# Kernel tuning notes

Hardware: AMD Instinct MI355X
Metric: run time of the kernel (lower is better)

Reference implementation:

```python
import jax, jax.numpy as jnp
import numpy as np

N = 50000          # nodes
E = 1_600_000      # edges (avg degree 32)
D_IN = 128
D_OUT = 128
K = 16             # SSGC hops
ALPHA = 0.05


def setup_inputs() -> dict:
    key = jax.random.key(0)
    k1, k2, k3 = jax.random.split(key, 3)
    node_emb = jax.random.normal(k1, (N, D_IN), dtype=jnp.float32)
    edge_index = jax.random.randint(k2, (2, E), 0, N, dtype=jnp.int32)
    # Parameters of SSGConv's internal Linear(in_channels, out_channels)
    weight = jax.random.normal(k3, (D_OUT, D_IN), dtype=jnp.float32) * (1.0 / np.sqrt(D_IN))
    bias = jnp.zeros((D_OUT,), dtype=jnp.float32)
    return {"node_emb": node_emb, "edge_index": edge_index, "weight": weight, "bias": bias}


def reference(node_emb, edge_index, weight, bias):
    n = node_emb.shape[0]
    # GCN normalization with self-loops (PyG gcn_norm, add_self_loops=True)
    loops = jnp.arange(n, dtype=edge_index.dtype)
    src = jnp.concatenate([edge_index[0], loops])  # [E+N]
    dst = jnp.concatenate([edge_index[1], loops])  # [E+N]
    ones = jnp.ones(src.shape[0], dtype=node_emb.dtype)
    deg = jax.ops.segment_sum(ones, dst, num_segments=n)           # in-degree incl. self-loop
    dinv = jnp.where(deg > 0, jax.lax.rsqrt(deg), 0.0)
    norm = dinv[src] * dinv[dst]                                   # [E+N]

    def prop(x):
        msgs = norm[:, None] * x[src]                              # [E+N, D]
        return jax.ops.segment_sum(msgs, dst, num_segments=n)

    # SSGConv: h = alpha*x0 + (1-alpha)/K * sum_{k=1..K} A_hat^k x0, then Linear
    def step(carry, _):
        x, h = carry
        x = prop(x)
        h = h + ((1.0 - ALPHA) / K) * x
        return (x, h), None

    (_, h), _ = jax.lax.scan(step, (node_emb, ALPHA * node_emb), None, length=K)
    out = h @ weight.T + bias
    # Dropout(p=0.5) is identity in eval mode
    return out
```

## Files before the change

### kernel.cpp

```cpp
#include <hip/hip_runtime.h>


#define N_NODES 50000
#define N_EDGES 1600000
#define D 128
#define K_HOPS 16
#define ALPHA 0.05f
#define HCOEF ((1.0f - ALPHA) / (float)K_HOPS)
#define NREP 8
#define N_SBLK ((N_NODES + 255) / 256)

#define DEG_IPT 8
#define REP_OF(i) (((i) >> 11) & (NREP - 1))

__device__ __forceinline__ unsigned int f2bf(float f) {
    unsigned int u = __float_as_uint(f);
    return (u + 0x7FFFu + ((u >> 16) & 1u)) >> 16;
}
__device__ __forceinline__ unsigned int pack_bf2(float x, float y) {
    return f2bf(x) | (f2bf(y) << 16);
}
__device__ __forceinline__ float bf_lo(unsigned int w) { return __uint_as_float(w << 16); }
__device__ __forceinline__ float bf_hi(unsigned int w) { return __uint_as_float(w & 0xFFFF0000u); }

__global__ void deg_kernel(const int* __restrict__ dst, int* __restrict__ degR,
                           int* __restrict__ rank, int e) {
    int gid = blockIdx.x * 256 + threadIdx.x;
    int i0 = gid * DEG_IPT;
    if (i0 >= e) return;
    int rep = REP_OF(i0);
    int* base = degR + rep * N_NODES;
    int4 d0 = *(const int4*)&dst[i0];
    int4 d1 = *(const int4*)&dst[i0 + 4];
    int r[8];
    r[0] = atomicAdd(&base[d0.x], 1);
    r[1] = atomicAdd(&base[d0.y], 1);
    r[2] = atomicAdd(&base[d0.z], 1);
    r[3] = atomicAdd(&base[d0.w], 1);
    r[4] = atomicAdd(&base[d1.x], 1);
    r[5] = atomicAdd(&base[d1.y], 1);
    r[6] = atomicAdd(&base[d1.z], 1);
    r[7] = atomicAdd(&base[d1.w], 1);
    *(int4*)&rank[i0]     = make_int4(r[0], r[1], r[2], r[3]);
    *(int4*)&rank[i0 + 4] = make_int4(r[4], r[5], r[6], r[7]);
}

__global__ void combine_kernel(int* __restrict__ degR, int* __restrict__ deg,
                               float* __restrict__ dinv, float* __restrict__ selfw, int n) {
    int i = blockIdx.x * 256 + threadIdx.x;
    if (i < n) {
        int run = 0;
        #pragma unroll
        for (int r = 0; r < NREP; ++r) {
            int v = degR[r * N_NODES + i];
            degR[r * N_NODES + i] = run;
            run += v;
        }
        deg[i] = run;
        float di = rsqrtf((float)(run + 1));
        dinv[i] = di;
        selfw[i] = di * di;
    }
}

__device__ __forceinline__ int block_scan_excl(int v) {
    __shared__ int ws[4];
    int tid = threadIdx.x, lane = tid & 63, wid = tid >> 6;
    int s = v;
    #pragma unroll
    for (int off = 1; off < 64; off <<= 1) {
        int t = __shfl_up(s, off, 64);
        if (lane >= off) s += t;
    }
    if (lane == 63) ws[wid] = s;
    __syncthreads();
    int woff = 0;
    #pragma unroll
    for (int w = 0; w < 3; ++w)
        if (w < wid) woff += ws[w];
    return woff + s - v;
}

__global__ void scan_part(const int* __restrict__ deg, int* __restrict__ part, int n) {
    int i = blockIdx.x * 256 + threadIdx.x;
    int v = (i < n) ? deg[i] : 0;
    #pragma unroll
    for (int off = 1; off < 64; off <<= 1) v += __shfl_xor(v, off, 64);
    __shared__ int ws[4];
    if ((threadIdx.x & 63) == 0) ws[threadIdx.x >> 6] = v;
    __syncthreads();
    if (threadIdx.x == 0) part[blockIdx.x] = ws[0] + ws[1] + ws[2] + ws[3];
}

__global__ void scan_mid(int* __restrict__ part, int nb) {
    int tid = threadIdx.x;
    int v = (tid < nb) ? part[tid] : 0;
    int e = block_scan_excl(v);
    if (tid < nb) part[tid] = e;
}

__global__ void scan_fin(const int* __restrict__ deg, const int* __restrict__ part,
                         int* __restrict__ row_start, int n) {
    int i = blockIdx.x * 256 + threadIdx.x;
    int v = (i < n) ? deg[i] : 0;
    int e = block_scan_excl(v) + part[blockIdx.x];
    if (i < n) row_start[i] = e;
    if (i == n - 1) row_start[n] = e + v;
}

__global__ void scatter_kernel(const int* __restrict__ src, const int* __restrict__ dst,
                               const int* __restrict__ rank, const int* __restrict__ row_start,
                               const int* __restrict__ pref, int2* __restrict__ csr,
                               const float* __restrict__ dinv, int e) {
    int gid = blockIdx.x * 256 + threadIdx.x;
    int i0 = gid * 4;
    if (i0 >= e) return;
    int4 dv = *(const int4*)&dst[i0];
    int4 sv = *(const int4*)&src[i0];
    int4 rv = *(const int4*)&rank[i0];
    int d[4] = {dv.x, dv.y, dv.z, dv.w};
    int s[4] = {sv.x, sv.y, sv.z, sv.w};
    int r[4] = {rv.x, rv.y, rv.z, rv.w};
    int pos[4];
    float w[4];
    #pragma unroll
    for (int q = 0; q < 4; ++q) {
        int rep = REP_OF(i0 + q);
        pos[q] = row_start[d[q]] + pref[rep * N_NODES + d[q]] + r[q];
        w[q] = dinv[d[q]] * dinv[s[q]];
    }
    #pragma unroll
    for (int q = 0; q < 4; ++q)
        csr[pos[q]] = make_int2(s[q], __float_as_int(w[q]));
}

__global__ void init_kernel(const float2* __restrict__ x0, unsigned int* __restrict__ xb,
                            float2* __restrict__ h, int n2) {
    int i = blockIdx.x * blockDim.x + threadIdx.x;
    if (i < n2) {
        float2 v = x0[i];
        xb[i] = pack_bf2(v.x, v.y);
        h[i] = make_float2(ALPHA * v.x, ALPHA * v.y);
    }
}

#define GATHER_BLOCK(W)                                                         \
    {                                                                           \
        unsigned int g[W];                                                      \
        float wv[W];                                                            \
        _Pragma("unroll") for (int q = 0; q < W; ++q) {                         \
            int s = __shfl(rec.x, j + q);                                       \
            wv[q] = __int_as_float(__shfl(rec.y, j + q));                       \
            g[q] = xb[(size_t)s * 64 + lane];                                   \
        }                                                                       \
        _Pragma("unroll") for (int q = 0; q < W; ++q) {                         \
            accx += wv[q] * bf_lo(g[q]);                                        \
            accy += wv[q] * bf_hi(g[q]);                                        \
        }                                                                       \
        j += W;                                                                 \
    }

__global__ __launch_bounds__(256) void agg_kernel(
    const unsigned int* __restrict__ xb, unsigned int* __restrict__ yb,
    float2* __restrict__ h2, const float* __restrict__ selfw,
    const int* __restrict__ row_start, const int2* __restrict__ csr, int update_h) {
    int wid = threadIdx.x >> 6;
    int lane = threadIdx.x & 63;
    int node = blockIdx.x * 4 + wid;
    if (node >= N_NODES) return;

    int r0 = row_start[node];
    int r1 = row_start[node + 1];
    int deg = r1 - r0;
    size_t o = (size_t)node * 64 + lane;

    unsigned int vw = xb[o];
    float sw = selfw[node];
    float accx = sw * bf_lo(vw), accy = sw * bf_hi(vw);

    for (int base = 0; base < deg; base += 64) {
        int cnt = deg - base;
        if (cnt > 64) cnt = 64;
        int idx = r0 + base + lane;
        if (idx >= r1) idx = r1 - 1;
        int2 rec = csr[idx];

        int j = 0;
        while (j + 16 <= cnt) GATHER_BLOCK(16);
        if (j + 8 <= cnt) GATHER_BLOCK(8);
        if (j + 4 <= cnt) GATHER_BLOCK(4);
        for (; j < cnt; ++j) {
            int s = __shfl(rec.x, j);
            float w = __int_as_float(__shfl(rec.y, j));
            unsigned int gw = xb[(size_t)s * 64 + lane];
            accx += w * bf_lo(gw);
            accy += w * bf_hi(gw);
        }
    }

    yb[o] = pack_bf2(accx, accy);
    if (update_h) {
        float2 hv = h2[o];
        hv.x += HCOEF * (bf_lo(vw) + accx);
        hv.y += HCOEF * (bf_hi(vw) + accy);
        h2[o] = hv;
    }
}

__global__ __launch_bounds__(256) void gemm_kernel(
    const float* __restrict__ h, const float* __restrict__ w,
    const float* __restrict__ bias, float* __restrict__ out) {
    __shared__ float sAT[128][64];
    __shared__ float sBT[128][64];
    int tid = threadIdx.x;
    int row0 = blockIdx.x * 64;
    int col0 = blockIdx.y * 64;

    for (int idx = tid; idx < 64 * 32; idx += 256) {
        int r = idx & 63, kq = idx >> 6;
        float4 v;
        if (row0 + r < N_NODES)
            v = *(const float4*)&h[(size_t)(row0 + r) * D + kq * 4];
        else
            v = make_float4(0.f, 0.f, 0.f, 0.f);
        sAT[kq * 4 + 0][r] = v.x;
        sAT[kq * 4 + 1][r] = v.y;
        sAT[kq * 4 + 2][r] = v.z;
        sAT[kq * 4 + 3][r] = v.w;
    }
    for (int idx = tid; idx < 64 * 32; idx += 256) {
        int c = idx & 63, kq = idx >> 6;
        float4 v = *(const float4*)&w[(size_t)(col0 + c) * D + kq * 4];
        sBT[kq * 4 + 0][c] = v.x;
        sBT[kq * 4 + 1][c] = v.y;
        sBT[kq * 4 + 2][c] = v.z;
        sBT[kq * 4 + 3][c] = v.w;
    }
    __syncthreads();

    int cg = tid & 15;
    int rg = tid >> 4;
    float acc[4][4] = {};
    #pragma unroll 2
    for (int k = 0; k < 128; ++k) {
        float4 a = *(const float4*)&sAT[k][rg * 4];
        float4 b = *(const float4*)&sBT[k][cg * 4];
        acc[0][0] += a.x * b.x; acc[0][1] += a.x * b.y; acc[0][2] += a.x * b.z; acc[0][3] += a.x * b.w;
        acc[1][0] += a.y * b.x; acc[1][1] += a.y * b.y; acc[1][2] += a.y * b.z; acc[1][3] += a.y * b.w;
        acc[2][0] += a.z * b.x; acc[2][1] += a.z * b.y; acc[2][2] += a.z * b.z; acc[2][3] += a.z * b.w;
        acc[3][0] += a.w * b.x; acc[3][1] += a.w * b.y; acc[3][2] += a.w * b.z; acc[3][3] += a.w * b.w;
    }

    float4 bv = *(const float4*)&bias[col0 + cg * 4];
    #pragma unroll
    for (int i = 0; i < 4; ++i) {
        int r = row0 + rg * 4 + i;
        if (r < N_NODES) {
            float4 ov = make_float4(acc[i][0] + bv.x, acc[i][1] + bv.y,
                                    acc[i][2] + bv.z, acc[i][3] + bv.w);
            *(float4*)&out[(size_t)r * D + col0 + cg * 4] = ov;
        }
    }
}

extern "C" void kernel_launch(void* const* d_in, const int* in_sizes, int n_in,
                              void* d_out, int out_size, void* d_ws, size_t ws_size,
                              hipStream_t stream) {
    const float* node_emb = (const float*)d_in[0];
    const int*   edge     = (const int*)d_in[1];
    const float* weight   = (const float*)d_in[2];
    const float* bias     = (const float*)d_in[3];
    float* out = (float*)d_out;

    char* ws = (char*)d_ws;
    float*        hbuf = (float*)ws;        ws += (size_t)N_NODES * D * sizeof(float);
    unsigned int* xb0  = (unsigned int*)ws; ws += (size_t)N_NODES * 64 * sizeof(unsigned int);
    unsigned int* xb1  = (unsigned int*)ws; ws += (size_t)N_NODES * 64 * sizeof(unsigned int);
    int2*  csr      = (int2*)ws;  ws += (size_t)N_EDGES * sizeof(int2);
    int*   rank     = (int*)ws;   ws += (size_t)N_EDGES * sizeof(int);
    int*   degR     = (int*)ws;   ws += (size_t)NREP * N_NODES * sizeof(int);
    int*   deg      = (int*)ws;   ws += (size_t)N_NODES * sizeof(int);
    int*   row_start= (int*)ws;   ws += (size_t)(N_NODES + 16) * sizeof(int);
    float* dinv     = (float*)ws; ws += (size_t)N_NODES * sizeof(float);
    float* selfw    = (float*)ws; ws += (size_t)N_NODES * sizeof(float);
    int*   part     = (int*)ws;   ws += 256 * sizeof(int);

    const int* srcp = edge;
    const int* dstp = edge + N_EDGES;

    hipMemsetAsync(degR, 0, (size_t)NREP * N_NODES * sizeof(int), stream);

    int deg_threads = N_EDGES / DEG_IPT;
    deg_kernel<<<(deg_threads + 255) / 256, 256, 0, stream>>>(dstp, degR, rank, N_EDGES);
    combine_kernel<<<(N_NODES + 255) / 256, 256, 0, stream>>>(degR, deg, dinv, selfw, N_NODES);
    scan_part<<<N_SBLK, 256, 0, stream>>>(deg, part, N_NODES);
    scan_mid<<<1, 256, 0, stream>>>(part, N_SBLK);
    scan_fin<<<N_SBLK, 256, 0, stream>>>(deg, part, row_start, N_NODES);
    int sc_threads = N_EDGES / 4;
    scatter_kernel<<<(sc_threads + 255) / 256, 256, 0, stream>>>(srcp, dstp, rank, row_start,
                                                                 degR, csr, dinv, N_EDGES);

    int n2 = N_NODES * D / 2;
    init_kernel<<<(n2 + 255) / 256, 256, 0, stream>>>((const float2*)node_emb, xb0,
                                                      (float2*)hbuf, n2);

    unsigned int* cur = xb0;
    unsigned int* nxt = xb1;
    for (int k = 0; k < K_HOPS; ++k) {
        agg_kernel<<<(N_NODES + 3) / 4, 256, 0, stream>>>(cur, nxt, (float2*)hbuf,
                                                          selfw, row_start, csr, k & 1);
        unsigned int* tmp = cur; cur = nxt; nxt = tmp;
    }

    dim3 ggrid((N_NODES + 63) / 64, 2);
    gemm_kernel<<<ggrid, 256, 0, stream>>>(hbuf, weight, bias, out);
}
```

Before: 1.072 ms.

## Restructure aggregation to 16-lane groups handling four nodes across column slices

The aggregation kernel no longer gives each node a full 64-lane wavefront. Each 16-lane group now processes four consecutive nodes, looping over four 16-word column slices, with shuffles of width 16 and a reduced grid. The aim is to cut wasted lanes and shuffle overhead and to raise memory-level parallelism per wave. In exchange, each gathered row is read as 64-byte segments across four separate passes, and each lane does four times as much sequential work, which may lower achieved bandwidth.

Result: slower. 2.022 ms (+88.6%).

```diff
diff --git a/kernel.cpp b/kernel.cpp
--- a/kernel.cpp
+++ b/kernel.cpp
@@ -12,6 +12,11 @@
 
 #define DEG_IPT 8
 #define REP_OF(i) (((i) >> 11) & (NREP - 1))
+
+#define GROUPS_PER_BLOCK 16
+#define N_GROUPS (N_NODES / 4)
+#define AGG_BLOCKS ((N_GROUPS + GROUPS_PER_BLOCK - 1) / GROUPS_PER_BLOCK)
+#define N_SLICES 4
 
 __device__ __forceinline__ unsigned int f2bf(float f) {
     unsigned int u = __float_as_uint(f);
@@ -144,18 +149,18 @@
     }
 }
 
-#define GATHER_BLOCK(W)                                                         \
+#define GATHER_G(W)                                                             \
     {                                                                           \
-        unsigned int g[W];                                                      \
+        unsigned int gg[W];                                                     \
         float wv[W];                                                            \
         _Pragma("unroll") for (int q = 0; q < W; ++q) {                         \
-            int s = __shfl(rec.x, j + q);                                       \
-            wv[q] = __int_as_float(__shfl(rec.y, j + q));                       \
-            g[q] = xb[(size_t)s * 64 + lane];                                   \
+            int ss = __shfl(rec.x, j + q, 16);                                  \
+            wv[q] = __int_as_float(__shfl(rec.y, j + q, 16));                   \
+            gg[q] = xb[(size_t)ss * 64 + soff];                                 \
         }                                                                       \
         _Pragma("unroll") for (int q = 0; q < W; ++q) {                         \
-            accx += wv[q] * bf_lo(g[q]);                                        \
-            accy += wv[q] * bf_hi(g[q]);                                        \
+            accx += wv[q] * bf_lo(gg[q]);                                       \
+            accy += wv[q] * bf_hi(gg[q]);                                       \
         }                                                                       \
         j += W;                                                                 \
     }
@@ -164,46 +169,51 @@
     const unsigned int* __restrict__ xb, unsigned int* __restrict__ yb,
     float2* __restrict__ h2, const float* __restrict__ selfw,
     const int* __restrict__ row_start, const int2* __restrict__ csr, int update_h) {
-    int wid = threadIdx.x >> 6;
-    int lane = threadIdx.x & 63;
-    int node = blockIdx.x * 4 + wid;
-    if (node >= N_NODES) return;
-
-    int r0 = row_start[node];
-    int r1 = row_start[node + 1];
-    int deg = r1 - r0;
-    size_t o = (size_t)node * 64 + lane;
-
-    unsigned int vw = xb[o];
-    float sw = selfw[node];
-    float accx = sw * bf_lo(vw), accy = sw * bf_hi(vw);
-
-    for (int base = 0; base < deg; base += 64) {
-        int cnt = deg - base;
-        if (cnt > 64) cnt = 64;
-        int idx = r0 + base + lane;
-        if (idx >= r1) idx = r1 - 1;
-        int2 rec = csr[idx];
-
-        int j = 0;
-        while (j + 16 <= cnt) GATHER_BLOCK(16);
-        if (j + 8 <= cnt) GATHER_BLOCK(8);
-        if (j + 4 <= cnt) GATHER_BLOCK(4);
-        for (; j < cnt; ++j) {
-            int s = __shfl(rec.x, j);
-            float w = __int_as_float(__shfl(rec.y, j));
-            unsigned int gw = xb[(size_t)s * 64 + lane];
-            accx += w * bf_lo(gw);
-            accy += w * bf_hi(gw);
+    int g = blockIdx.x * GROUPS_PER_BLOCK + (threadIdx.x >> 4);
+    int sub = threadIdx.x & 15;
+    if (g >= N_GROUPS) return;
+    int n0 = g * 4;
+
+    for (int s = 0; s < N_SLICES; ++s) {
+        int soff = s * 16 + sub;
+        #pragma unroll
+        for (int ni = 0; ni < 4; ++ni) {
+            int node = n0 + ni;
+            int r0 = row_start[node];
+            int r1 = row_start[node + 1];
+            size_t o = (size_t)node * 64 + soff;
+
+            unsigned int vw = xb[o];
+            float sw = selfw[node];
+            float accx = sw * bf_lo(vw), accy = sw * bf_hi(vw);
+
+            for (int base = r0; base < r1; base += 16) {
+                int cnt = r1 - base;
+                if (cnt > 16) cnt = 16;
+                int idx = base + sub;
+                if (idx >= r1) idx = r1 - 1;
+                int2 rec = csr[idx];
+
+                int j = 0;
+                while (j + 8 <= cnt) GATHER_G(8);
+                if (j + 4 <= cnt) GATHER_G(4);
+                for (; j < cnt; ++j) {
+                    int ss = __shfl(rec.x, j, 16);
+                    float w = __int_as_float(__shfl(rec.y, j, 16));
+                    unsigned int gw = xb[(size_t)ss * 64 + soff];
+                    accx += w * bf_lo(gw);
+                    accy += w * bf_hi(gw);
+                }
+            }
+
+            yb[o] = pack_bf2(accx, accy);
+            if (update_h) {
+                float2 hv = h2[o];
+                hv.x += HCOEF * (bf_lo(vw) + accx);
+                hv.y += HCOEF * (bf_hi(vw) + accy);
+                h2[o] = hv;
+            }
         }
-    }
-
-    yb[o] = pack_bf2(accx, accy);
-    if (update_h) {
-        float2 hv = h2[o];
-        hv.x += HCOEF * (bf_lo(vw) + accx);
-        hv.y += HCOEF * (bf_hi(vw) + accy);
-        h2[o] = hv;
     }
 }
 
@@ -307,8 +317,8 @@
     unsigned int* cur = xb0;
     unsigned int* nxt = xb1;
     for (int k = 0; k < K_HOPS; ++k) {
-        agg_kernel<<<(N_NODES + 3) / 4, 256, 0, stream>>>(cur, nxt, (float2*)hbuf,
-                                                          selfw, row_start, csr, k & 1);
+        agg_kernel<<<AGG_BLOCKS, 256, 0, stream>>>(cur, nxt, (float2*)hbuf,
+                                                   selfw, row_start, csr, k & 1);
         unsigned int* tmp = cur; cur = nxt; nxt = tmp;
     }
 
```

## Slice bf16 feature matrix into four 64-byte column slices for gather locality

Applied to the files above, without the earlier changes.

The bf16 node features are stored as four column slices of 32 dims each, so each slice of the whole graph is 50000 x 64 bytes. The aggregation grid runs slice by slice, so the working set of one pass stays small enough to live in cache. Within a wavefront, four 16-lane groups each process different edges, and a cross-lane reduction combines them at the end. The edge list is now read four times per hop, and nontemporal loads and stores are added for the CSR, output and h traffic.

New measurement: 1.792 ms. 1.67x slower.

```diff
diff --git a/kernel.cpp b/kernel.cpp
--- a/kernel.cpp
+++ b/kernel.cpp
@@ -12,6 +12,10 @@
 
 #define DEG_IPT 8
 #define REP_OF(i) (((i) >> 11) & (NREP - 1))
+
+#define N_SLICES 4
+#define SLICE_STRIDE ((size_t)N_NODES * 16)
+#define BLOCKS_PER_SLICE (N_NODES / 4)
 
 __device__ __forceinline__ unsigned int f2bf(float f) {
     unsigned int u = __float_as_uint(f);
@@ -134,76 +138,99 @@
         csr[pos[q]] = make_int2(s[q], __float_as_int(w[q]));
 }
 
-__global__ void init_kernel(const float2* __restrict__ x0, unsigned int* __restrict__ xb,
+__global__ void init_kernel(const float2* __restrict__ x0, unsigned int* __restrict__ xbs,
                             float2* __restrict__ h, int n2) {
     int i = blockIdx.x * blockDim.x + threadIdx.x;
     if (i < n2) {
         float2 v = x0[i];
-        xb[i] = pack_bf2(v.x, v.y);
+        int node = i >> 6, d = i & 63;
+        int slice = d >> 4, sub = d & 15;
+        xbs[(size_t)slice * SLICE_STRIDE + (size_t)node * 16 + sub] = pack_bf2(v.x, v.y);
         h[i] = make_float2(ALPHA * v.x, ALPHA * v.y);
     }
 }
 
-#define GATHER_BLOCK(W)                                                         \
+#define GFULL(W)                                                                \
     {                                                                           \
-        unsigned int g[W];                                                      \
+        unsigned int gv[W];                                                     \
         float wv[W];                                                            \
-        _Pragma("unroll") for (int q = 0; q < W; ++q) {                         \
-            int s = __shfl(rec.x, j + q);                                       \
-            wv[q] = __int_as_float(__shfl(rec.y, j + q));                       \
-            g[q] = xb[(size_t)s * 64 + lane];                                   \
+        _Pragma("unroll") for (int q = 0; q < (W); ++q) {                       \
+            int e4 = 4 * (t + q) + grp;                                         \
+            int ss = __shfl(recs, e4);                                          \
+            wv[q] = __int_as_float(__shfl(recw, e4));                           \
+            gv[q] = xs[(size_t)ss * 16 + sub];                                  \
         }                                                                       \
-        _Pragma("unroll") for (int q = 0; q < W; ++q) {                         \
-            accx += wv[q] * bf_lo(g[q]);                                        \
-            accy += wv[q] * bf_hi(g[q]);                                        \
+        _Pragma("unroll") for (int q = 0; q < (W); ++q) {                       \
+            accx += wv[q] * bf_lo(gv[q]);                                       \
+            accy += wv[q] * bf_hi(gv[q]);                                       \
         }                                                                       \
-        j += W;                                                                 \
+        t += (W);                                                               \
     }
 
 __global__ __launch_bounds__(256) void agg_kernel(
-    const unsigned int* __restrict__ xb, unsigned int* __restrict__ yb,
+    const unsigned int* __restrict__ xbs, unsigned int* __restrict__ ybs,
     float2* __restrict__ h2, const float* __restrict__ selfw,
     const int* __restrict__ row_start, const int2* __restrict__ csr, int update_h) {
     int wid = threadIdx.x >> 6;
     int lane = threadIdx.x & 63;
-    int node = blockIdx.x * 4 + wid;
-    if (node >= N_NODES) return;
-
+    int grp = lane >> 4, sub = lane & 15;
+    int bid = blockIdx.x;
+    int slice = bid / BLOCKS_PER_SLICE;
+    int node = (bid % BLOCKS_PER_SLICE) * 4 + wid;
+
+    const unsigned int* xs = xbs + (size_t)slice * SLICE_STRIDE;
     int r0 = row_start[node];
     int r1 = row_start[node + 1];
-    int deg = r1 - r0;
-    size_t o = (size_t)node * 64 + lane;
-
-    unsigned int vw = xb[o];
-    float sw = selfw[node];
-    float accx = sw * bf_lo(vw), accy = sw * bf_hi(vw);
-
-    for (int base = 0; base < deg; base += 64) {
-        int cnt = deg - base;
+    int dg = r1 - r0;
+
+    float accx = 0.f, accy = 0.f;
+
+    for (int base = 0; base < dg; base += 64) {
+        int cnt = dg - base;
         if (cnt > 64) cnt = 64;
         int idx = r0 + base + lane;
         if (idx >= r1) idx = r1 - 1;
-        int2 rec = csr[idx];
-
-        int j = 0;
-        while (j + 16 <= cnt) GATHER_BLOCK(16);
-        if (j + 8 <= cnt) GATHER_BLOCK(8);
-        if (j + 4 <= cnt) GATHER_BLOCK(4);
-        for (; j < cnt; ++j) {
-            int s = __shfl(rec.x, j);
-            float w = __int_as_float(__shfl(rec.y, j));
-            unsigned int gw = xb[(size_t)s * 64 + lane];
+        long long rr = __builtin_nontemporal_load((const long long*)&csr[idx]);
+        int recs = (int)rr;
+        int recw = (int)(rr >> 32);
+
+        int nf = cnt >> 2;
+        int t = 0;
+        while (t + 8 <= nf) GFULL(8);
+        if (t + 4 <= nf) GFULL(4);
+        while (t < nf) GFULL(1);
+        if (cnt & 3) {
+            int e4 = 4 * nf + grp;
+            int ss = __shfl(recs, e4);
+            float w = __int_as_float(__shfl(recw, e4));
+            if (e4 >= cnt) w = 0.f;
+            unsigned int gw = xs[(size_t)ss * 16 + sub];
             accx += w * bf_lo(gw);
             accy += w * bf_hi(gw);
         }
     }
 
-    yb[o] = pack_bf2(accx, accy);
-    if (update_h) {
-        float2 hv = h2[o];
-        hv.x += HCOEF * (bf_lo(vw) + accx);
-        hv.y += HCOEF * (bf_hi(vw) + accy);
-        h2[o] = hv;
+    accx += __shfl_xor(accx, 16, 64);
+    accx += __shfl_xor(accx, 32, 64);
+    accy += __shfl_xor(accy, 16, 64);
+    accy += __shfl_xor(accy, 32, 64);
+
+    if (grp == 0) {
+        unsigned int vw = xs[(size_t)node * 16 + sub];
+        float sw = selfw[node];
+        float xl = bf_lo(vw), xh = bf_hi(vw);
+        accx += sw * xl;
+        accy += sw * xh;
+        size_t so = (size_t)slice * SLICE_STRIDE + (size_t)node * 16 + sub;
+        __builtin_nontemporal_store(pack_bf2(accx, accy), &ybs[so]);
+        if (update_h) {
+            size_t ho = (size_t)node * 64 + slice * 16 + sub;
+            union { long long ll; float2 f; } hu;
+            hu.ll = __builtin_nontemporal_load((const long long*)&h2[ho]);
+            hu.f.x += HCOEF * (xl + accx);
+            hu.f.y += HCOEF * (xh + accy);
+            __builtin_nontemporal_store(hu.ll, (long long*)&h2[ho]);
+        }
     }
 }
 
@@ -307,8 +334,8 @@
     unsigned int* cur = xb0;
     unsigned int* nxt = xb1;
     for (int k = 0; k < K_HOPS; ++k) {
-        agg_kernel<<<(N_NODES + 3) / 4, 256, 0, stream>>>(cur, nxt, (float2*)hbuf,
-                                                          selfw, row_start, csr, k & 1);
+        agg_kernel<<<N_SLICES * BLOCKS_PER_SLICE, 256, 0, stream>>>(
+            cur, nxt, (float2*)hbuf, selfw, row_start, csr, k & 1);
         unsigned int* tmp = cur; cur = nxt; nxt = tmp;
     }
 
```
